# Performance work log

Hardware: AMD Instinct MI355X
Metric: run time of the kernel (lower is better)

Reference implementation:

```python
import jax, jax.numpy as jnp
import numpy as np

N_ENTITY = 64368
N_REL = 40
DIM = 128
N_BASES = 8
N_EDGES = 500000
BATCH = 64
SEED_LEN = 32


def _glorot(k, shape, gain=1.414):
    fan_in, fan_out = shape[0], shape[1]
    bound = gain * np.sqrt(6.0 / (fan_in + fan_out))
    return jax.random.uniform(k, shape, jnp.float32, -bound, bound)


def setup_inputs() -> dict:
    key = jax.random.key(0)
    ks = jax.random.split(key, 11)
    return dict(
        seed_ids=jax.random.randint(ks[0], (BATCH, SEED_LEN), 0, N_ENTITY),
        edge_src=jax.random.randint(ks[1], (N_EDGES,), 0, N_ENTITY),
        edge_dst=jax.random.randint(ks[2], (N_EDGES,), 0, N_ENTITY),
        edge_type=jax.random.randint(ks[3], (N_EDGES,), 0, N_REL),
        basis=jax.random.normal(ks[4], (N_BASES, N_ENTITY, DIM), jnp.float32) * 0.02,
        att=jax.random.normal(ks[5], (N_REL, N_BASES), jnp.float32) * 0.1,
        root=jax.random.normal(ks[6], (N_ENTITY, DIM), jnp.float32) * 0.02,
        rgcn_bias=jnp.zeros((DIM,), jnp.float32),
        attn_a=_glorot(ks[7], (DIM, DIM)),
        attn_b=_glorot(ks[8], (DIM, 1)),
        out_bias=jnp.zeros((N_ENTITY,), jnp.float32),
    )


def _rgcn_nodes(basis, att, root, rgcn_bias, edge_src, edge_dst, edge_type):
    # RGCNConv with x=None: message for edge e is row src[e] of w[type[e]],
    # where w = att @ basis (basis decomposition); 'mean' aggregation to dst;
    # update: aggr + root + bias.
    n_entity, dim = root.shape
    coeff = att[edge_type]  # [E, nb]
    agg = jnp.zeros((n_entity, dim), jnp.float32)
    for b in range(basis.shape[0]):  # small fixed loop over bases
        m = basis[b][edge_src] * coeff[:, b][:, None]  # [E, dim]
        agg = agg + jax.ops.segment_sum(m, edge_dst, num_segments=n_entity)
    deg = jax.ops.segment_sum(jnp.ones_like(edge_dst, jnp.float32), edge_dst,
                              num_segments=n_entity)
    agg = agg / jnp.maximum(deg, 1.0)[:, None]
    return agg + root + rgcn_bias[None, :]


def reference(seed_ids, edge_src, edge_dst, edge_type, basis, att, root,
              rgcn_bias, attn_a, attn_b, out_bias):
    nodes = _rgcn_nodes(basis, att, root, rgcn_bias, edge_src, edge_dst, edge_type)
    # self-attention pooling over each seed set (all entries valid / non-empty)
    H = nodes[seed_ids]  # [B, S, D]
    e = jnp.einsum('bsd,d->bs', jnp.tanh(jnp.einsum('bsd,de->bse', H, attn_a)),
                   attn_b[:, 0])  # [B, S]
    attn = jax.nn.softmax(e, axis=-1)
    u = jnp.einsum('bs,bsd->bd', attn, H)  # [B, D]
    # scores = F.linear(u, nodes_features, output.bias)
    scores = u @ nodes.T + out_bias[None, :]  # [B, n_entity]
    return scores
```

## Files before the change

### kernel.cpp

```cpp
#include <hip/hip_runtime.h>
#include <hip/hip_bf16.h>
#include <hip/hip_fp16.h>

#define N_ENTITY 64368
#define N_REL 40
#define DIM 128
#define N_BASES 8
#define N_EDGES 500000
#define BATCH 64
#define SEED_LEN 32
#define NROWS (BATCH * SEED_LEN)
#define SCAN_NB ((N_ENTITY + 255) / 256)
#define NPAD (SCAN_NB * 256)

struct alignas(8) half4 { __half2 lo, hi; };

__global__ __launch_bounds__(256) void k_hist2(
    const int* __restrict__ edst, const int* __restrict__ esrc,
    int* __restrict__ hist2)
{
    int e = blockIdx.x * 256 + threadIdx.x;
    if (e < N_EDGES) {
        atomicAdd(&hist2[edst[e]], 1);
        atomicAdd(&hist2[NPAD + esrc[e]], 1);
    }
}

__global__ __launch_bounds__(256) void k_scan1(
    const int* __restrict__ hist2, int* __restrict__ ptr2,
    int* __restrict__ partial)
{
    __shared__ int s[256];
    int tid = threadIdx.x;
    int gid = blockIdx.x * 256 + tid;
    int v = hist2[gid];
    s[tid] = v;
    __syncthreads();
    for (int off = 1; off < 256; off <<= 1) {
        int t = (tid >= off) ? s[tid - off] : 0;
        __syncthreads();
        s[tid] += t;
        __syncthreads();
    }
    ptr2[gid] = s[tid] - v;
    if (tid == 255) partial[blockIdx.x] = s[255];
}

__global__ __launch_bounds__(256) void k_scan2(
    const int* __restrict__ partial, int* __restrict__ poff)
{
    __shared__ int s[256];
    int tid = threadIdx.x;
    int base = blockIdx.x * SCAN_NB;
    int v = (tid < SCAN_NB) ? partial[base + tid] : 0;
    s[tid] = v;
    __syncthreads();
    for (int off = 1; off < 256; off <<= 1) {
        int t = (tid >= off) ? s[tid - off] : 0;
        __syncthreads();
        s[tid] += t;
        __syncthreads();
    }
    if (tid < SCAN_NB) poff[base + tid] = s[tid] - v;
}

__global__ __launch_bounds__(256) void k_scan3(
    int* __restrict__ ptr2, const int* __restrict__ poff,
    int* __restrict__ work2)
{
    int gid = blockIdx.x * 256 + threadIdx.x;
    int p = ptr2[gid] + poff[blockIdx.x];
    ptr2[gid] = p;
    work2[gid] = p;
}

__global__ __launch_bounds__(256) void k_scatter2(
    const int* __restrict__ esrc, const int* __restrict__ edst,
    const int* __restrict__ etype, int* __restrict__ work2,
    int* __restrict__ ptype, int* __restrict__ idx)
{
    int e = blockIdx.x * 256 + threadIdx.x;
    if (e < N_EDGES) {
        int spos = atomicAdd(&work2[NPAD + esrc[e]], 1);
        int dpos = atomicAdd(&work2[edst[e]], 1);
        ptype[spos] = etype[e];
        idx[dpos] = spos;
    }
}

__global__ __launch_bounds__(256) void k_scatterD(
    const int* __restrict__ esrc, const int* __restrict__ edst,
    const int* __restrict__ etype, int* __restrict__ work2,
    int* __restrict__ meta)
{
    int e = blockIdx.x * 256 + threadIdx.x;
    if (e < N_EDGES) {
        int pos = atomicAdd(&work2[edst[e]], 1);
        meta[pos] = esrc[e] * 64 + etype[e];
    }
}

__global__ __launch_bounds__(256) void k_phaseA(
    const int* __restrict__ sptr, const int* __restrict__ shist,
    const int* __restrict__ ptype, const float* __restrict__ basis,
    const float* __restrict__ att, __half* __restrict__ msg)
{
    __shared__ float att_s[N_REL * N_BASES];
    int tid = threadIdx.x;
    for (int i = tid; i < N_REL * N_BASES; i += 256) att_s[i] = att[i];
    __syncthreads();

    int sid = (blockIdx.x * 256 + tid) >> 5;
    int l32 = tid & 31;
    if (sid >= N_ENTITY) return;
    int cnt = shist[sid];
    if (cnt == 0) return;
    int p = sptr[sid];

    const size_t bstride = (size_t)N_ENTITY * DIM;
    const float* bp = basis + (size_t)sid * DIM + l32 * 4;
    float4 r0 = *(const float4*)(bp + 0 * bstride);
    float4 r1 = *(const float4*)(bp + 1 * bstride);
    float4 r2 = *(const float4*)(bp + 2 * bstride);
    float4 r3 = *(const float4*)(bp + 3 * bstride);
    float4 r4 = *(const float4*)(bp + 4 * bstride);
    float4 r5 = *(const float4*)(bp + 5 * bstride);
    float4 r6 = *(const float4*)(bp + 6 * bstride);
    float4 r7 = *(const float4*)(bp + 7 * bstride);

    int j = 0;
    for (; j + 1 < cnt; j += 2) {
        int tA = ptype[p + j];
        int tB = ptype[p + j + 1];
        const float* cA = att_s + tA * N_BASES;
        const float* cB = att_s + tB * N_BASES;
        float4 cA0 = *(const float4*)(cA);
        float4 cA1 = *(const float4*)(cA + 4);
        float4 cB0 = *(const float4*)(cB);
        float4 cB1 = *(const float4*)(cB + 4);

        float4 mA, mB;
        mA.x = cA0.x*r0.x + cA0.y*r1.x + cA0.z*r2.x + cA0.w*r3.x
             + cA1.x*r4.x + cA1.y*r5.x + cA1.z*r6.x + cA1.w*r7.x;
        mA.y = cA0.x*r0.y + cA0.y*r1.y + cA0.z*r2.y + cA0.w*r3.y
             + cA1.x*r4.y + cA1.y*r5.y + cA1.z*r6.y + cA1.w*r7.y;
        mA.z = cA0.x*r0.z + cA0.y*r1.z + cA0.z*r2.z + cA0.w*r3.z
             + cA1.x*r4.z + cA1.y*r5.z + cA1.z*r6.z + cA1.w*r7.z;
        mA.w = cA0.x*r0.w + cA0.y*r1.w + cA0.z*r2.w + cA0.w*r3.w
             + cA1.x*r4.w + cA1.y*r5.w + cA1.z*r6.w + cA1.w*r7.w;
        mB.x = cB0.x*r0.x + cB0.y*r1.x + cB0.z*r2.x + cB0.w*r3.x
             + cB1.x*r4.x + cB1.y*r5.x + cB1.z*r6.x + cB1.w*r7.x;
        mB.y = cB0.x*r0.y + cB0.y*r1.y + cB0.z*r2.y + cB0.w*r3.y
             + cB1.x*r4.y + cB1.y*r5.y + cB1.z*r6.y + cB1.w*r7.y;
        mB.z = cB0.x*r0.z + cB0.y*r1.z + cB0.z*r2.z + cB0.w*r3.z
             + cB1.x*r4.z + cB1.y*r5.z + cB1.z*r6.z + cB1.w*r7.z;
        mB.w = cB0.x*r0.w + cB0.y*r1.w + cB0.z*r2.w + cB0.w*r3.w
             + cB1.x*r4.w + cB1.y*r5.w + cB1.z*r6.w + cB1.w*r7.w;

        half4 hA, hB;
        hA.lo = __floats2half2_rn(mA.x, mA.y);
        hA.hi = __floats2half2_rn(mA.z, mA.w);
        hB.lo = __floats2half2_rn(mB.x, mB.y);
        hB.hi = __floats2half2_rn(mB.z, mB.w);
        *(half4*)(msg + ((size_t)(p + j)     << 7) + (l32 << 2)) = hA;
        *(half4*)(msg + ((size_t)(p + j + 1) << 7) + (l32 << 2)) = hB;
    }
    if (j < cnt) {
        int tA = ptype[p + j];
        const float* cA = att_s + tA * N_BASES;
        float4 cA0 = *(const float4*)(cA);
        float4 cA1 = *(const float4*)(cA + 4);
        float4 mA;
        mA.x = cA0.x*r0.x + cA0.y*r1.x + cA0.z*r2.x + cA0.w*r3.x
             + cA1.x*r4.x + cA1.y*r5.x + cA1.z*r6.x + cA1.w*r7.x;
        mA.y = cA0.x*r0.y + cA0.y*r1.y + cA0.z*r2.y + cA0.w*r3.y
             + cA1.x*r4.y + cA1.y*r5.y + cA1.z*r6.y + cA1.w*r7.y;
        mA.z = cA0.x*r0.z + cA0.y*r1.z + cA0.z*r2.z + cA0.w*r3.z
             + cA1.x*r4.z + cA1.y*r5.z + cA1.z*r6.z + cA1.w*r7.z;
        mA.w = cA0.x*r0.w + cA0.y*r1.w + cA0.z*r2.w + cA0.w*r3.w
             + cA1.x*r4.w + cA1.y*r5.w + cA1.z*r6.w + cA1.w*r7.w;
        half4 hA;
        hA.lo = __floats2half2_rn(mA.x, mA.y);
        hA.hi = __floats2half2_rn(mA.z, mA.w);
        *(half4*)(msg + ((size_t)(p + j) << 7) + (l32 << 2)) = hA;
    }
}

__global__ __launch_bounds__(256) void k_phaseB(
    const int* __restrict__ dptr, const int* __restrict__ dhist,
    const int* __restrict__ idx, const __half* __restrict__ msg,
    const float* __restrict__ root, const float* __restrict__ bias,
    float* __restrict__ agg)
{
    int wid  = (int)((blockIdx.x * 256 + threadIdx.x) >> 6);
    int lane = threadIdx.x & 63;
    if (wid >= N_ENTITY) return;
    int cnt = dhist[wid];
    int p   = dptr[wid];
    const __half2* mp = (const __half2*)msg;

    float ax = 0.f, ay = 0.f;
    int j = 0;
    for (; j + 3 < cnt; j += 4) {
        int i0 = idx[p + j + 0];
        int i1 = idx[p + j + 1];
        int i2 = idx[p + j + 2];
        int i3 = idx[p + j + 3];
        __half2 v0 = mp[((size_t)i0 << 6) + lane];
        __half2 v1 = mp[((size_t)i1 << 6) + lane];
        __half2 v2 = mp[((size_t)i2 << 6) + lane];
        __half2 v3 = mp[((size_t)i3 << 6) + lane];
        float2 f0 = __half22float2(v0);
        float2 f1 = __half22float2(v1);
        float2 f2 = __half22float2(v2);
        float2 f3 = __half22float2(v3);
        ax += (f0.x + f1.x) + (f2.x + f3.x);
        ay += (f0.y + f1.y) + (f2.y + f3.y);
    }
    for (; j < cnt; ++j) {
        int i0 = idx[p + j];
        float2 f = __half22float2(mp[((size_t)i0 << 6) + lane]);
        ax += f.x; ay += f.y;
    }

    float inv = 1.0f / fmaxf((float)cnt, 1.0f);
    int o = wid * DIM + lane * 2;
    float2 r  = *(const float2*)(root + o);
    float2 bb = *(const float2*)(bias + lane * 2);
    float2 outv;
    outv.x = ax * inv + r.x + bb.x;
    outv.y = ay * inv + r.y + bb.y;
    *(float2*)(agg + o) = outv;
}

#define ACC8(C0, C1, V0, V1, V2, V3, V4, V5, V6, V7)                         \
    acc.x += C0.x*V0.x + C0.y*V1.x + C0.z*V2.x + C0.w*V3.x                   \
           + C1.x*V4.x + C1.y*V5.x + C1.z*V6.x + C1.w*V7.x;                  \
    acc.y += C0.x*V0.y + C0.y*V1.y + C0.z*V2.y + C0.w*V3.y                   \
           + C1.x*V4.y + C1.y*V5.y + C1.z*V6.y + C1.w*V7.y;                  \
    acc.z += C0.x*V0.z + C0.y*V1.z + C0.z*V2.z + C0.w*V3.z                   \
           + C1.x*V4.z + C1.y*V5.z + C1.z*V6.z + C1.w*V7.z;                  \
    acc.w += C0.x*V0.w + C0.y*V1.w + C0.z*V2.w + C0.w*V3.w                   \
           + C1.x*V4.w + C1.y*V5.w + C1.z*V6.w + C1.w*V7.w;

__global__ __launch_bounds__(256) void k_gather(
    const int* __restrict__ ptr, const int* __restrict__ hist,
    const int* __restrict__ meta, const float* __restrict__ basis,
    const float* __restrict__ att, const float* __restrict__ root,
    const float* __restrict__ bias, float* __restrict__ agg)
{
    __shared__ float att_s[N_REL * N_BASES];
    int tid = threadIdx.x;
    for (int i = tid; i < N_REL * N_BASES; i += 256) att_s[i] = att[i];
    __syncthreads();

    int wid  = (int)((blockIdx.x * 256 + tid) >> 6);
    int lane = tid & 63;
    if (wid >= N_ENTITY) return;

    int half = lane >> 5;
    int l32  = lane & 31;
    int p   = ptr[wid];
    int cnt = hist[wid];
    const size_t bstride = (size_t)N_ENTITY * DIM;

    float4 acc = {0.f, 0.f, 0.f, 0.f};
    int j = 0;
    for (; j + 3 < cnt; j += 4) {
        int mA0 = meta[p + j + 0];
        int mA1 = meta[p + j + 1];
        int mB0 = meta[p + j + 2];
        int mB1 = meta[p + j + 3];
        int mA = half ? mA1 : mA0;
        int mB = half ? mB1 : mB0;
        const float* bA = basis + (size_t)(mA >> 6) * DIM + l32 * 4;
        const float* bB = basis + (size_t)(mB >> 6) * DIM + l32 * 4;
        float4 a0 = *(const float4*)(bA + 0 * bstride);
        float4 a1 = *(const float4*)(bA + 1 * bstride);
        float4 a2 = *(const float4*)(bA + 2 * bstride);
        float4 a3 = *(const float4*)(bA + 3 * bstride);
        float4 a4 = *(const float4*)(bA + 4 * bstride);
        float4 a5 = *(const float4*)(bA + 5 * bstride);
        float4 a6 = *(const float4*)(bA + 6 * bstride);
        float4 a7 = *(const float4*)(bA + 7 * bstride);
        float4 b0 = *(const float4*)(bB + 0 * bstride);
        float4 b1 = *(const float4*)(bB + 1 * bstride);
        float4 b2 = *(const float4*)(bB + 2 * bstride);
        float4 b3 = *(const float4*)(bB + 3 * bstride);
        float4 b4 = *(const float4*)(bB + 4 * bstride);
        float4 b5 = *(const float4*)(bB + 5 * bstride);
        float4 b6 = *(const float4*)(bB + 6 * bstride);
        float4 b7 = *(const float4*)(bB + 7 * bstride);
        float4 cA0 = *(const float4*)(att_s + (mA & 63) * N_BASES);
        float4 cA1 = *(const float4*)(att_s + (mA & 63) * N_BASES + 4);
        float4 cB0 = *(const float4*)(att_s + (mB & 63) * N_BASES);
        float4 cB1 = *(const float4*)(att_s + (mB & 63) * N_BASES + 4);
        ACC8(cA0, cA1, a0, a1, a2, a3, a4, a5, a6, a7)
        ACC8(cB0, cB1, b0, b1, b2, b3, b4, b5, b6, b7)
    }
    for (; j < cnt; j += 2) {
        int m0 = meta[p + j];
        bool has1 = (j + 1 < cnt);
        int m1 = has1 ? meta[p + j + 1] : m0;
        int m = half ? m1 : m0;
        float sc = (half && !has1) ? 0.0f : 1.0f;
        const float* bA = basis + (size_t)(m >> 6) * DIM + l32 * 4;
        float4 a0 = *(const float4*)(bA + 0 * bstride);
        float4 a1 = *(const float4*)(bA + 1 * bstride);
        float4 a2 = *(const float4*)(bA + 2 * bstride);
        float4 a3 = *(const float4*)(bA + 3 * bstride);
        float4 a4 = *(const float4*)(bA + 4 * bstride);
        float4 a5 = *(const float4*)(bA + 5 * bstride);
        float4 a6 = *(const float4*)(bA + 6 * bstride);
        float4 a7 = *(const float4*)(bA + 7 * bstride);
        float4 c0 = *(const float4*)(att_s + (m & 63) * N_BASES);
        float4 c1 = *(const float4*)(att_s + (m & 63) * N_BASES + 4);
        c0.x *= sc; c0.y *= sc; c0.z *= sc; c0.w *= sc;
        c1.x *= sc; c1.y *= sc; c1.z *= sc; c1.w *= sc;
        ACC8(c0, c1, a0, a1, a2, a3, a4, a5, a6, a7)
    }

    acc.x += __shfl_xor(acc.x, 32, 64);
    acc.y += __shfl_xor(acc.y, 32, 64);
    acc.z += __shfl_xor(acc.z, 32, 64);
    acc.w += __shfl_xor(acc.w, 32, 64);

    if (half == 0) {
        float inv = 1.0f / fmaxf((float)cnt, 1.0f);
        int o = wid * DIM + l32 * 4;
        float4 r  = *(const float4*)(root + o);
        float4 bb = *(const float4*)(bias + l32 * 4);
        float4 outv;
        outv.x = acc.x * inv + r.x + bb.x;
        outv.y = acc.y * inv + r.y + bb.y;
        outv.z = acc.z * inv + r.z + bb.z;
        outv.w = acc.w * inv + r.w + bb.w;
        *(float4*)(agg + o) = outv;
    }
}

__global__ __launch_bounds__(256) void k_attn_gemm(
    const int* __restrict__ seed_ids, const float* __restrict__ nodes,
    const float* __restrict__ A, float* __restrict__ T)
{
    __shared__ float As[DIM * 132];
    __shared__ float Hs[16 * DIM];

    int tid = threadIdx.x;
    int r0  = blockIdx.x * 16;

    for (int i = tid; i < DIM * DIM; i += 256) {
        int row = i >> 7, col = i & 127;
        As[row * 132 + col] = A[i];
    }
    for (int i = tid; i < 16 * DIM; i += 256) {
        int rr = i >> 7, d = i & 127;
        int nid = seed_ids[r0 + rr];
        Hs[rr * DIM + d] = nodes[(size_t)nid * DIM + d];
    }
    __syncthreads();

    int jx = tid & 31;
    int iy = tid >> 5;
    float acc[2][4] = {{0,0,0,0},{0,0,0,0}};

    for (int d = 0; d < DIM; ++d) {
        float h0 = Hs[(iy * 2 + 0) * DIM + d];
        float h1 = Hs[(iy * 2 + 1) * DIM + d];
        const float4 a4 = *(const float4*)(As + d * 132 + jx * 4);
        acc[0][0] += h0 * a4.x; acc[0][1] += h0 * a4.y;
        acc[0][2] += h0 * a4.z; acc[0][3] += h0 * a4.w;
        acc[1][0] += h1 * a4.x; acc[1][1] += h1 * a4.y;
        acc[1][2] += h1 * a4.z; acc[1][3] += h1 * a4.w;
    }
    #pragma unroll
    for (int i = 0; i < 2; ++i) {
        int r = r0 + iy * 2 + i;
        #pragma unroll
        for (int k = 0; k < 4; ++k)
            T[(size_t)r * DIM + jx * 4 + k] = tanhf(acc[i][k]);
    }
}

__global__ __launch_bounds__(256) void k_attn_pool(
    const int* __restrict__ seed_ids, const float* __restrict__ nodes,
    const float* __restrict__ T, const float* __restrict__ Bv,
    float* __restrict__ u, float* __restrict__ uT)
{
    __shared__ float part[SEED_LEN][9];
    __shared__ float attw[SEED_LEN];

    int b = blockIdx.x, tid = threadIdx.x;
    int s = tid >> 3, g = tid & 7;

    float pe = 0.0f;
    for (int jj = g; jj < DIM; jj += 8)
        pe += T[(size_t)(b * SEED_LEN + s) * DIM + jj] * Bv[jj];
    part[s][g] = pe;
    __syncthreads();

    if (tid < SEED_LEN) {
        float e = 0.0f;
        for (int k = 0; k < 8; ++k) e += part[tid][k];
        attw[tid] = e;
    }
    __syncthreads();

    if (tid == 0) {
        float mx = -1e30f;
        for (int k = 0; k < SEED_LEN; ++k) mx = fmaxf(mx, attw[k]);
        float ssum = 0.0f;
        for (int k = 0; k < SEED_LEN; ++k) {
            float v = expf(attw[k] - mx);
            attw[k] = v; ssum += v;
        }
        float inv = 1.0f / ssum;
        for (int k = 0; k < SEED_LEN; ++k) attw[k] *= inv;
    }
    __syncthreads();

    if (tid < DIM) {
        float acc = 0.0f;
        for (int k = 0; k < SEED_LEN; ++k) {
            int nid = seed_ids[b * SEED_LEN + k];
            acc += attw[k] * nodes[(size_t)nid * DIM + tid];
        }
        u[b * DIM + tid]  = acc;
        uT[tid * BATCH + b] = acc;
    }
}

__global__ __launch_bounds__(256) void k_scores(
    const float* __restrict__ nodes, const float* __restrict__ uT,
    const float* __restrict__ out_bias, float* __restrict__ out)
{
    __shared__ float Nl[DIM * 65];

    int tid = threadIdx.x;
    int n0  = blockIdx.x * 64;

    for (int i = tid; i < 64 * DIM; i += 256) {
        int n = i >> 7, d = i & 127;
        int gn = n0 + n;
        Nl[d * 65 + n] = (gn < N_ENTITY) ? nodes[(size_t)gn * DIM + d] : 0.0f;
    }
    __syncthreads();

    int w    = __builtin_amdgcn_readfirstlane(tid >> 6);
    int lane = tid & 63;
    int b0   = w * 16;

    float acc[16];
    #pragma unroll
    for (int k = 0; k < 16; ++k) acc[k] = 0.0f;

    #pragma unroll 4
    for (int d = 0; d < DIM; ++d) {
        float nv = Nl[d * 65 + lane];
        const float* up = uT + d * BATCH + b0;
        #pragma unroll
        for (int k = 0; k < 16; ++k) acc[k] += up[k] * nv;
    }

    int gn = n0 + lane;
    if (gn < N_ENTITY) {
        float ob = out_bias[gn];
        #pragma unroll
        for (int k = 0; k < 16; ++k)
            out[(size_t)(b0 + k) * N_ENTITY + gn] = acc[k] + ob;
    }
}

extern "C" void kernel_launch(void* const* d_in, const int* in_sizes, int n_in,
                              void* d_out, int out_size, void* d_ws, size_t ws_size,
                              hipStream_t stream)
{
    const int*   seed_ids  = (const int*)d_in[0];
    const int*   esrc      = (const int*)d_in[1];
    const int*   edst      = (const int*)d_in[2];
    const int*   etype     = (const int*)d_in[3];
    const float* basis     = (const float*)d_in[4];
    const float* att       = (const float*)d_in[5];
    const float* root      = (const float*)d_in[6];
    const float* rgcn_bias = (const float*)d_in[7];
    const float* attn_a    = (const float*)d_in[8];
    const float* attn_b    = (const float*)d_in[9];
    const float* out_bias  = (const float*)d_in[10];
    float* out = (float*)d_out;

    const size_t AGG_F  = (size_t)N_ENTITY * DIM;
    const size_t MSG_W  = (size_t)N_EDGES * 64;
    const size_t H2_I   = (size_t)2 * NPAD;

    const size_t main_words = AGG_F + MSG_W + 3 * H2_I + 1024
                            + 2 * (size_t)N_EDGES + (size_t)NROWS * DIM
                            + 2 * BATCH * DIM;
    bool big = ws_size >= main_words * 4;

    if (big) {
        float*  agg    = (float*)d_ws;
        __half* msg    = (__half*)(agg + AGG_F);
        int*    hist2  = (int*)(agg + AGG_F + MSG_W);
        int*    ptr2   = hist2 + H2_I;
        int*    work2  = ptr2 + H2_I;
        int*    part2  = work2 + H2_I;
        int*    poff2  = part2 + 512;
        int*    ptype  = poff2 + 512;
        int*    idx    = ptype + N_EDGES;
        float*  T      = (float*)(idx + N_EDGES);
        float*  u      = T + (size_t)NROWS * DIM;
        float*  uT     = u + BATCH * DIM;

        hipMemsetAsync(hist2, 0, H2_I * sizeof(int), stream);
        k_hist2<<<(N_EDGES + 255) / 256, 256, 0, stream>>>(edst, esrc, hist2);
        k_scan1<<<2 * SCAN_NB, 256, 0, stream>>>(hist2, ptr2, part2);
        k_scan2<<<2, 256, 0, stream>>>(part2, poff2);
        k_scan3<<<2 * SCAN_NB, 256, 0, stream>>>(ptr2, poff2, work2);
        k_scatter2<<<(N_EDGES + 255) / 256, 256, 0, stream>>>(
            esrc, edst, etype, work2, ptype, idx);

        k_phaseA<<<N_ENTITY / 8, 256, 0, stream>>>(
            ptr2 + NPAD, hist2 + NPAD, ptype, basis, att, msg);
        k_phaseB<<<N_ENTITY / 4, 256, 0, stream>>>(
            ptr2, hist2, idx, msg, root, rgcn_bias, agg);

        k_attn_gemm<<<NROWS / 16, 256, 0, stream>>>(seed_ids, agg, attn_a, T);
        k_attn_pool<<<BATCH, 256, 0, stream>>>(seed_ids, agg, T, attn_b, u, uT);
        k_scores<<<(N_ENTITY + 63) / 64, 256, 0, stream>>>(agg, uT, out_bias, out);
    } else {
        float* agg     = (float*)d_ws;
        int*   hist2   = (int*)(agg + AGG_F);
        int*   ptr2    = hist2 + H2_I;
        int*   work2   = ptr2 + H2_I;
        int*   part2   = work2 + H2_I;
        int*   poff2   = part2 + 512;
        int*   meta    = poff2 + 512;
        float* T       = (float*)(meta + N_EDGES);
        float* u       = T + (size_t)NROWS * DIM;
        float* uT      = u + BATCH * DIM;

        hipMemsetAsync(hist2, 0, H2_I * sizeof(int), stream);
        k_hist2<<<(N_EDGES + 255) / 256, 256, 0, stream>>>(edst, esrc, hist2);
        k_scan1<<<2 * SCAN_NB, 256, 0, stream>>>(hist2, ptr2, part2);
        k_scan2<<<2, 256, 0, stream>>>(part2, poff2);
        k_scan3<<<2 * SCAN_NB, 256, 0, stream>>>(ptr2, poff2, work2);
        k_scatterD<<<(N_EDGES + 255) / 256, 256, 0, stream>>>(
            esrc, edst, etype, work2, meta);

        k_gather<<<(N_ENTITY * 64 + 255) / 256, 256, 0, stream>>>(
            ptr2, hist2, meta, basis, att, root, rgcn_bias, agg);

        k_attn_gemm<<<NROWS / 16, 256, 0, stream>>>(seed_ids, agg, attn_a, T);
        k_attn_pool<<<BATCH, 256, 0, stream>>>(seed_ids, agg, T, attn_b, u, uT);
        k_scores<<<(N_ENTITY + 63) / 64, 256, 0, stream>>>(agg, uT, out_bias, out);
    }
}
```

Before: 612.2 us.

## Fuse RGCN pipeline into one cooperative persistent kernel and merge attention kernels

The memset, histogram, three scan kernels, scatter and both message phases are replaced by a single cooperative kernel with 1024 persistent blocks that separates the stages with grid-wide syncs. This removes the launch gaps and the separate memset. The scan offset step now has each chunk re-sum its preceding partials directly. The attention GEMM and the pooling kernel are merged into one per-batch kernel that keeps H in shared memory, which removes the T buffer round trip. In exchange, grid.sync has its own cost and the grid-stride loops run at lower parallelism than the original full-size grids.

```diff
diff --git a/kernel.cpp b/kernel.cpp
--- a/kernel.cpp
+++ b/kernel.cpp
@@ -1,6 +1,8 @@
 #include <hip/hip_runtime.h>
-#include <hip/hip_bf16.h>
 #include <hip/hip_fp16.h>
+#include <hip/hip_cooperative_groups.h>
+
+namespace cg = cooperative_groups;
 
 #define N_ENTITY 64368
 #define N_REL 40
@@ -12,10 +14,321 @@
 #define NROWS (BATCH * SEED_LEN)
 #define SCAN_NB ((N_ENTITY + 255) / 256)
 #define NPAD (SCAN_NB * 256)
+#define G_COOP 1024
 
 struct alignas(8) half4 { __half2 lo, hi; };
 
-__global__ __launch_bounds__(256) void k_hist2(
+__global__ __launch_bounds__(256, 4) void k_rgcn_all(
+    const int* __restrict__ esrc, const int* __restrict__ edst,
+    const int* __restrict__ etype, const float* __restrict__ basis,
+    const float* __restrict__ att, const float* __restrict__ root,
+    const float* __restrict__ bias,
+    int* __restrict__ hist2, int* __restrict__ ptr2, int* __restrict__ work2,
+    int* __restrict__ part2, int* __restrict__ ptype, int* __restrict__ idx,
+    __half* __restrict__ msg, float* __restrict__ agg)
+{
+    cg::grid_group grid = cg::this_grid();
+    __shared__ int s[256];
+    __shared__ float att_s[N_REL * N_BASES];
+
+    const int tid = threadIdx.x;
+    const int bid = blockIdx.x;
+    const int G   = gridDim.x;
+    const int gsz = G * 256;
+    const int gid = bid * 256 + tid;
+
+    for (int i = gid; i < 2 * NPAD; i += gsz) hist2[i] = 0;
+    for (int i = tid; i < N_REL * N_BASES; i += 256) att_s[i] = att[i];
+    __threadfence();
+    grid.sync();
+
+    for (int e = gid; e < N_EDGES; e += gsz) {
+        atomicAdd(&hist2[edst[e]], 1);
+        atomicAdd(&hist2[NPAD + esrc[e]], 1);
+    }
+    __threadfence();
+    grid.sync();
+
+    for (int c = bid; c < 2 * SCAN_NB; c += G) {
+        int v = hist2[c * 256 + tid];
+        s[tid] = v;
+        __syncthreads();
+        for (int off = 1; off < 256; off <<= 1) {
+            int t = (tid >= off) ? s[tid - off] : 0;
+            __syncthreads();
+            s[tid] += t;
+            __syncthreads();
+        }
+        ptr2[c * 256 + tid] = s[tid] - v;
+        if (tid == 255) part2[c] = s[255];
+        __syncthreads();
+    }
+    __threadfence();
+    grid.sync();
+
+    for (int c = bid; c < 2 * SCAN_NB; c += G) {
+        int cstart = (c < SCAN_NB) ? 0 : SCAN_NB;
+        int sum = 0;
+        for (int k = cstart + tid; k < c; k += 256) sum += part2[k];
+        s[tid] = sum;
+        __syncthreads();
+        for (int off = 128; off > 0; off >>= 1) {
+            if (tid < off) s[tid] += s[tid + off];
+            __syncthreads();
+        }
+        int p = ptr2[c * 256 + tid] + s[0];
+        ptr2[c * 256 + tid]  = p;
+        work2[c * 256 + tid] = p;
+        __syncthreads();
+    }
+    __threadfence();
+    grid.sync();
+
+    for (int e = gid; e < N_EDGES; e += gsz) {
+        int spos = atomicAdd(&work2[NPAD + esrc[e]], 1);
+        int dpos = atomicAdd(&work2[edst[e]], 1);
+        ptype[spos] = etype[e];
+        idx[dpos]   = spos;
+    }
+    __threadfence();
+    grid.sync();
+
+    {
+        const int l32 = tid & 31;
+        const int* sptr  = ptr2 + NPAD;
+        const int* shist = hist2 + NPAD;
+        const size_t bstride = (size_t)N_ENTITY * DIM;
+
+        for (int sid = (bid << 3) + (tid >> 5); sid < N_ENTITY; sid += (G << 3)) {
+            int cnt = shist[sid];
+            if (cnt == 0) continue;
+            int p = sptr[sid];
+
+            const float* bp = basis + (size_t)sid * DIM + l32 * 4;
+            float4 r0 = *(const float4*)(bp + 0 * bstride);
+            float4 r1 = *(const float4*)(bp + 1 * bstride);
+            float4 r2 = *(const float4*)(bp + 2 * bstride);
+            float4 r3 = *(const float4*)(bp + 3 * bstride);
+            float4 r4 = *(const float4*)(bp + 4 * bstride);
+            float4 r5 = *(const float4*)(bp + 5 * bstride);
+            float4 r6 = *(const float4*)(bp + 6 * bstride);
+            float4 r7 = *(const float4*)(bp + 7 * bstride);
+
+            int j = 0;
+            for (; j + 1 < cnt; j += 2) {
+                int tA = ptype[p + j];
+                int tB = ptype[p + j + 1];
+                const float* cA = att_s + tA * N_BASES;
+                const float* cB = att_s + tB * N_BASES;
+                float4 cA0 = *(const float4*)(cA);
+                float4 cA1 = *(const float4*)(cA + 4);
+                float4 cB0 = *(const float4*)(cB);
+                float4 cB1 = *(const float4*)(cB + 4);
+
+                float4 mA, mB;
+                mA.x = cA0.x*r0.x + cA0.y*r1.x + cA0.z*r2.x + cA0.w*r3.x
+                     + cA1.x*r4.x + cA1.y*r5.x + cA1.z*r6.x + cA1.w*r7.x;
+                mA.y = cA0.x*r0.y + cA0.y*r1.y + cA0.z*r2.y + cA0.w*r3.y
+                     + cA1.x*r4.y + cA1.y*r5.y + cA1.z*r6.y + cA1.w*r7.y;
+                mA.z = cA0.x*r0.z + cA0.y*r1.z + cA0.z*r2.z + cA0.w*r3.z
+                     + cA1.x*r4.z + cA1.y*r5.z + cA1.z*r6.z + cA1.w*r7.z;
+                mA.w = cA0.x*r0.w + cA0.y*r1.w + cA0.z*r2.w + cA0.w*r3.w
+                     + cA1.x*r4.w + cA1.y*r5.w + cA1.z*r6.w + cA1.w*r7.w;
+                mB.x = cB0.x*r0.x + cB0.y*r1.x + cB0.z*r2.x + cB0.w*r3.x
+                     + cB1.x*r4.x + cB1.y*r5.x + cB1.z*r6.x + cB1.w*r7.x;
+                mB.y = cB0.x*r0.y + cB0.y*r1.y + cB0.z*r2.y + cB0.w*r3.y
+                     + cB1.x*r4.y + cB1.y*r5.y + cB1.z*r6.y + cB1.w*r7.y;
+                mB.z = cB0.x*r0.z + cB0.y*r1.z + cB0.z*r2.z + cB0.w*r3.z
+                     + cB1.x*r4.z + cB1.y*r5.z + cB1.z*r6.z + cB1.w*r7.z;
+                mB.w = cB0.x*r0.w + cB0.y*r1.w + cB0.z*r2.w + cB0.w*r3.w
+                     + cB1.x*r4.w + cB1.y*r5.w + cB1.z*r6.w + cB1.w*r7.w;
+
+                half4 hA, hB;
+                hA.lo = __floats2half2_rn(mA.x, mA.y);
+                hA.hi = __floats2half2_rn(mA.z, mA.w);
+                hB.lo = __floats2half2_rn(mB.x, mB.y);
+                hB.hi = __floats2half2_rn(mB.z, mB.w);
+                *(half4*)(msg + ((size_t)(p + j)     << 7) + (l32 << 2)) = hA;
+                *(half4*)(msg + ((size_t)(p + j + 1) << 7) + (l32 << 2)) = hB;
+            }
+            if (j < cnt) {
+                int tA = ptype[p + j];
+                const float* cA = att_s + tA * N_BASES;
+                float4 cA0 = *(const float4*)(cA);
+                float4 cA1 = *(const float4*)(cA + 4);
+                float4 mA;
+                mA.x = cA0.x*r0.x + cA0.y*r1.x + cA0.z*r2.x + cA0.w*r3.x
+                     + cA1.x*r4.x + cA1.y*r5.x + cA1.z*r6.x + cA1.w*r7.x;
+                mA.y = cA0.x*r0.y + cA0.y*r1.y + cA0.z*r2.y + cA0.w*r3.y
+                     + cA1.x*r4.y + cA1.y*r5.y + cA1.z*r6.y + cA1.w*r7.y;
+                mA.z = cA0.x*r0.z + cA0.y*r1.z + cA0.z*r2.z + cA0.w*r3.z
+                     + cA1.x*r4.z + cA1.y*r5.z + cA1.z*r6.z + cA1.w*r7.z;
+                mA.w = cA0.x*r0.w + cA0.y*r1.w + cA0.z*r2.w + cA0.w*r3.w
+                     + cA1.x*r4.w + cA1.y*r5.w + cA1.z*r6.w + cA1.w*r7.w;
+                half4 hA;
+                hA.lo = __floats2half2_rn(mA.x, mA.y);
+                hA.hi = __floats2half2_rn(mA.z, mA.w);
+                *(half4*)(msg + ((size_t)(p + j) << 7) + (l32 << 2)) = hA;
+            }
+        }
+    }
+    __threadfence();
+    grid.sync();
+
+    {
+        const int lane = tid & 63;
+        const __half2* mp = (const __half2*)msg;
+
+        for (int wid = (bid << 2) + (tid >> 6); wid < N_ENTITY; wid += (G << 2)) {
+            int cnt = hist2[wid];
+            int p   = ptr2[wid];
+
+            float ax = 0.f, ay = 0.f;
+            int j = 0;
+            for (; j + 3 < cnt; j += 4) {
+                int i0 = idx[p + j + 0];
+                int i1 = idx[p + j + 1];
+                int i2 = idx[p + j + 2];
+                int i3 = idx[p + j + 3];
+                float2 f0 = __half22float2(mp[((size_t)i0 << 6) + lane]);
+                float2 f1 = __half22float2(mp[((size_t)i1 << 6) + lane]);
+                float2 f2 = __half22float2(mp[((size_t)i2 << 6) + lane]);
+                float2 f3 = __half22float2(mp[((size_t)i3 << 6) + lane]);
+                ax += (f0.x + f1.x) + (f2.x + f3.x);
+                ay += (f0.y + f1.y) + (f2.y + f3.y);
+            }
+            for (; j < cnt; ++j) {
+                int i0 = idx[p + j];
+                float2 f = __half22float2(mp[((size_t)i0 << 6) + lane]);
+                ax += f.x; ay += f.y;
+            }
+
+            float inv = 1.0f / fmaxf((float)cnt, 1.0f);
+            int o = wid * DIM + lane * 2;
+            float2 r  = *(const float2*)(root + o);
+            float2 bb = *(const float2*)(bias + lane * 2);
+            float2 outv;
+            outv.x = ax * inv + r.x + bb.x;
+            outv.y = ay * inv + r.y + bb.y;
+            *(float2*)(agg + o) = outv;
+        }
+    }
+}
+
+__global__ __launch_bounds__(256) void k_attn(
+    const int* __restrict__ seed_ids, const float* __restrict__ nodes,
+    const float* __restrict__ A, const float* __restrict__ Bv,
+    float* __restrict__ u, float* __restrict__ uT)
+{
+    __shared__ float Hs[SEED_LEN * DIM];
+    __shared__ float ew[SEED_LEN];
+    __shared__ float attw[SEED_LEN];
+
+    int b = blockIdx.x, tid = threadIdx.x;
+
+    for (int i = tid; i < SEED_LEN * DIM; i += 256) {
+        int ss = i >> 7, d = i & 127;
+        Hs[i] = nodes[(size_t)seed_ids[b * SEED_LEN + ss] * DIM + d];
+    }
+    __syncthreads();
+
+    int jx = tid & 31;
+    int iy = tid >> 5;
+    float acc[4][4] = {{0,0,0,0},{0,0,0,0},{0,0,0,0},{0,0,0,0}};
+
+    for (int d = 0; d < DIM; ++d) {
+        const float4 a4 = *(const float4*)(A + d * DIM + jx * 4);
+        float h0 = Hs[(iy * 4 + 0) * DIM + d];
+        float h1 = Hs[(iy * 4 + 1) * DIM + d];
+        float h2 = Hs[(iy * 4 + 2) * DIM + d];
+        float h3 = Hs[(iy * 4 + 3) * DIM + d];
+        acc[0][0] += h0 * a4.x; acc[0][1] += h0 * a4.y;
+        acc[0][2] += h0 * a4.z; acc[0][3] += h0 * a4.w;
+        acc[1][0] += h1 * a4.x; acc[1][1] += h1 * a4.y;
+        acc[1][2] += h1 * a4.z; acc[1][3] += h1 * a4.w;
+        acc[2][0] += h2 * a4.x; acc[2][1] += h2 * a4.y;
+        acc[2][2] += h2 * a4.z; acc[2][3] += h2 * a4.w;
+        acc[3][0] += h3 * a4.x; acc[3][1] += h3 * a4.y;
+        acc[3][2] += h3 * a4.z; acc[3][3] += h3 * a4.w;
+    }
+
+    const float4 bv = *(const float4*)(Bv + jx * 4);
+    #pragma unroll
+    for (int i = 0; i < 4; ++i) {
+        float pe = tanhf(acc[i][0]) * bv.x + tanhf(acc[i][1]) * bv.y
+                 + tanhf(acc[i][2]) * bv.z + tanhf(acc[i][3]) * bv.w;
+        pe += __shfl_xor(pe, 1, 64);
+        pe += __shfl_xor(pe, 2, 64);
+        pe += __shfl_xor(pe, 4, 64);
+        pe += __shfl_xor(pe, 8, 64);
+        pe += __shfl_xor(pe, 16, 64);
+        if (jx == 0) ew[iy * 4 + i] = pe;
+    }
+    __syncthreads();
+
+    if (tid == 0) {
+        float mx = -1e30f;
+        for (int k = 0; k < SEED_LEN; ++k) mx = fmaxf(mx, ew[k]);
+        float ssum = 0.0f;
+        for (int k = 0; k < SEED_LEN; ++k) {
+            float v = expf(ew[k] - mx);
+            attw[k] = v; ssum += v;
+        }
+        float inv = 1.0f / ssum;
+        for (int k = 0; k < SEED_LEN; ++k) attw[k] *= inv;
+    }
+    __syncthreads();
+
+    if (tid < DIM) {
+        float a = 0.0f;
+        for (int k = 0; k < SEED_LEN; ++k) a += attw[k] * Hs[k * DIM + tid];
+        u[b * DIM + tid]  = a;
+        uT[tid * BATCH + b] = a;
+    }
+}
+
+__global__ __launch_bounds__(256) void k_scores(
+    const float* __restrict__ nodes, const float* __restrict__ uT,
+    const float* __restrict__ out_bias, float* __restrict__ out)
+{
+    __shared__ float Nl[DIM * 65];
+
+    int tid = threadIdx.x;
+    int n0  = blockIdx.x * 64;
+
+    for (int i = tid; i < 64 * DIM; i += 256) {
+        int n = i >> 7, d = i & 127;
+        int gn = n0 + n;
+        Nl[d * 65 + n] = (gn < N_ENTITY) ? nodes[(size_t)gn * DIM + d] : 0.0f;
+    }
+    __syncthreads();
+
+    int w    = __builtin_amdgcn_readfirstlane(tid >> 6);
+    int lane = tid & 63;
+    int b0   = w * 16;
+
+    float acc[16];
+    #pragma unroll
+    for (int k = 0; k < 16; ++k) acc[k] = 0.0f;
+
+    #pragma unroll 4
+    for (int d = 0; d < DIM; ++d) {
+        float nv = Nl[d * 65 + lane];
+        const float* up = uT + d * BATCH + b0;
+        #pragma unroll
+        for (int k = 0; k < 16; ++k) acc[k] += up[k] * nv;
+    }
+
+    int gn = n0 + lane;
+    if (gn < N_ENTITY) {
+        float ob = out_bias[gn];
+        #pragma unroll
+        for (int k = 0; k < 16; ++k)
+            out[(size_t)(b0 + k) * N_ENTITY + gn] = acc[k] + ob;
+    }
+}
+
+__global__ __launch_bounds__(256) void k_hist2F(
     const int* __restrict__ edst, const int* __restrict__ esrc,
     int* __restrict__ hist2)
 {
@@ -26,7 +339,7 @@
     }
 }
 
-__global__ __launch_bounds__(256) void k_scan1(
+__global__ __launch_bounds__(256) void k_scan1F(
     const int* __restrict__ hist2, int* __restrict__ ptr2,
     int* __restrict__ partial)
 {
@@ -46,7 +359,7 @@
     if (tid == 255) partial[blockIdx.x] = s[255];
 }
 
-__global__ __launch_bounds__(256) void k_scan2(
+__global__ __launch_bounds__(256) void k_scan2F(
     const int* __restrict__ partial, int* __restrict__ poff)
 {
     __shared__ int s[256];
@@ -64,7 +377,7 @@
     if (tid < SCAN_NB) poff[base + tid] = s[tid] - v;
 }
 
-__global__ __launch_bounds__(256) void k_scan3(
+__global__ __launch_bounds__(256) void k_scan3F(
     int* __restrict__ ptr2, const int* __restrict__ poff,
     int* __restrict__ work2)
 {
@@ -74,20 +387,6 @@
     work2[gid] = p;
 }
 
-__global__ __launch_bounds__(256) void k_scatter2(
-    const int* __restrict__ esrc, const int* __restrict__ edst,
-    const int* __restrict__ etype, int* __restrict__ work2,
-    int* __restrict__ ptype, int* __restrict__ idx)
-{
-    int e = blockIdx.x * 256 + threadIdx.x;
-    if (e < N_EDGES) {
-        int spos = atomicAdd(&work2[NPAD + esrc[e]], 1);
-        int dpos = atomicAdd(&work2[edst[e]], 1);
-        ptype[spos] = etype[e];
-        idx[dpos] = spos;
-    }
-}
-
 __global__ __launch_bounds__(256) void k_scatterD(
     const int* __restrict__ esrc, const int* __restrict__ edst,
     const int* __restrict__ etype, int* __restrict__ work2,
@@ -98,139 +397,6 @@
         int pos = atomicAdd(&work2[edst[e]], 1);
         meta[pos] = esrc[e] * 64 + etype[e];
     }
-}
-
-__global__ __launch_bounds__(256) void k_phaseA(
-    const int* __restrict__ sptr, const int* __restrict__ shist,
-    const int* __restrict__ ptype, const float* __restrict__ basis,
-    const float* __restrict__ att, __half* __restrict__ msg)
-{
-    __shared__ float att_s[N_REL * N_BASES];
-    int tid = threadIdx.x;
-    for (int i = tid; i < N_REL * N_BASES; i += 256) att_s[i] = att[i];
-    __syncthreads();
-
-    int sid = (blockIdx.x * 256 + tid) >> 5;
-    int l32 = tid & 31;
-    if (sid >= N_ENTITY) return;
-    int cnt = shist[sid];
-    if (cnt == 0) return;
-    int p = sptr[sid];
-
-    const size_t bstride = (size_t)N_ENTITY * DIM;
-    const float* bp = basis + (size_t)sid * DIM + l32 * 4;
-    float4 r0 = *(const float4*)(bp + 0 * bstride);
-    float4 r1 = *(const float4*)(bp + 1 * bstride);
-    float4 r2 = *(const float4*)(bp + 2 * bstride);
-    float4 r3 = *(const float4*)(bp + 3 * bstride);
-    float4 r4 = *(const float4*)(bp + 4 * bstride);
-    float4 r5 = *(const float4*)(bp + 5 * bstride);
-    float4 r6 = *(const float4*)(bp + 6 * bstride);
-    float4 r7 = *(const float4*)(bp + 7 * bstride);
-
-    int j = 0;
-    for (; j + 1 < cnt; j += 2) {
-        int tA = ptype[p + j];
-        int tB = ptype[p + j + 1];
-        const float* cA = att_s + tA * N_BASES;
-        const float* cB = att_s + tB * N_BASES;
-        float4 cA0 = *(const float4*)(cA);
-        float4 cA1 = *(const float4*)(cA + 4);
-        float4 cB0 = *(const float4*)(cB);
-        float4 cB1 = *(const float4*)(cB + 4);
-
-        float4 mA, mB;
-        mA.x = cA0.x*r0.x + cA0.y*r1.x + cA0.z*r2.x + cA0.w*r3.x
-             + cA1.x*r4.x + cA1.y*r5.x + cA1.z*r6.x + cA1.w*r7.x;
-        mA.y = cA0.x*r0.y + cA0.y*r1.y + cA0.z*r2.y + cA0.w*r3.y
-             + cA1.x*r4.y + cA1.y*r5.y + cA1.z*r6.y + cA1.w*r7.y;
-        mA.z = cA0.x*r0.z + cA0.y*r1.z + cA0.z*r2.z + cA0.w*r3.z
-             + cA1.x*r4.z + cA1.y*r5.z + cA1.z*r6.z + cA1.w*r7.z;
-        mA.w = cA0.x*r0.w + cA0.y*r1.w + cA0.z*r2.w + cA0.w*r3.w
-             + cA1.x*r4.w + cA1.y*r5.w + cA1.z*r6.w + cA1.w*r7.w;
-        mB.x = cB0.x*r0.x + cB0.y*r1.x + cB0.z*r2.x + cB0.w*r3.x
-             + cB1.x*r4.x + cB1.y*r5.x + cB1.z*r6.x + cB1.w*r7.x;
-        mB.y = cB0.x*r0.y + cB0.y*r1.y + cB0.z*r2.y + cB0.w*r3.y
-             + cB1.x*r4.y + cB1.y*r5.y + cB1.z*r6.y + cB1.w*r7.y;
-        mB.z = cB0.x*r0.z + cB0.y*r1.z + cB0.z*r2.z + cB0.w*r3.z
-             + cB1.x*r4.z + cB1.y*r5.z + cB1.z*r6.z + cB1.w*r7.z;
-        mB.w = cB0.x*r0.w + cB0.y*r1.w + cB0.z*r2.w + cB0.w*r3.w
-             + cB1.x*r4.w + cB1.y*r5.w + cB1.z*r6.w + cB1.w*r7.w;
-
-        half4 hA, hB;
-        hA.lo = __floats2half2_rn(mA.x, mA.y);
-        hA.hi = __floats2half2_rn(mA.z, mA.w);
-        hB.lo = __floats2half2_rn(mB.x, mB.y);
-        hB.hi = __floats2half2_rn(mB.z, mB.w);
-        *(half4*)(msg + ((size_t)(p + j)     << 7) + (l32 << 2)) = hA;
-        *(half4*)(msg + ((size_t)(p + j + 1) << 7) + (l32 << 2)) = hB;
-    }
-    if (j < cnt) {
-        int tA = ptype[p + j];
-        const float* cA = att_s + tA * N_BASES;
-        float4 cA0 = *(const float4*)(cA);
-        float4 cA1 = *(const float4*)(cA + 4);
-        float4 mA;
-        mA.x = cA0.x*r0.x + cA0.y*r1.x + cA0.z*r2.x + cA0.w*r3.x
-             + cA1.x*r4.x + cA1.y*r5.x + cA1.z*r6.x + cA1.w*r7.x;
-        mA.y = cA0.x*r0.y + cA0.y*r1.y + cA0.z*r2.y + cA0.w*r3.y
-             + cA1.x*r4.y + cA1.y*r5.y + cA1.z*r6.y + cA1.w*r7.y;
-        mA.z = cA0.x*r0.z + cA0.y*r1.z + cA0.z*r2.z + cA0.w*r3.z
-             + cA1.x*r4.z + cA1.y*r5.z + cA1.z*r6.z + cA1.w*r7.z;
-        mA.w = cA0.x*r0.w + cA0.y*r1.w + cA0.z*r2.w + cA0.w*r3.w
-             + cA1.x*r4.w + cA1.y*r5.w + cA1.z*r6.w + cA1.w*r7.w;
-        half4 hA;
-        hA.lo = __floats2half2_rn(mA.x, mA.y);
-        hA.hi = __floats2half2_rn(mA.z, mA.w);
-        *(half4*)(msg + ((size_t)(p + j) << 7) + (l32 << 2)) = hA;
-    }
-}
-
-__global__ __launch_bounds__(256) void k_phaseB(
-    const int* __restrict__ dptr, const int* __restrict__ dhist,
-    const int* __restrict__ idx, const __half* __restrict__ msg,
-    const float* __restrict__ root, const float* __restrict__ bias,
-    float* __restrict__ agg)
-{
-    int wid  = (int)((blockIdx.x * 256 + threadIdx.x) >> 6);
-    int lane = threadIdx.x & 63;
-    if (wid >= N_ENTITY) return;
-    int cnt = dhist[wid];
-    int p   = dptr[wid];
-    const __half2* mp = (const __half2*)msg;
-
-    float ax = 0.f, ay = 0.f;
-    int j = 0;
-    for (; j + 3 < cnt; j += 4) {
-        int i0 = idx[p + j + 0];
-        int i1 = idx[p + j + 1];
-        int i2 = idx[p + j + 2];
-        int i3 = idx[p + j + 3];
-        __half2 v0 = mp[((size_t)i0 << 6) + lane];
-        __half2 v1 = mp[((size_t)i1 << 6) + lane];
-        __half2 v2 = mp[((size_t)i2 << 6) + lane];
-        __half2 v3 = mp[((size_t)i3 << 6) + lane];
-        float2 f0 = __half22float2(v0);
-        float2 f1 = __half22float2(v1);
-        float2 f2 = __half22float2(v2);
-        float2 f3 = __half22float2(v3);
-        ax += (f0.x + f1.x) + (f2.x + f3.x);
-        ay += (f0.y + f1.y) + (f2.y + f3.y);
-    }
-    for (; j < cnt; ++j) {
-        int i0 = idx[p + j];
-        float2 f = __half22float2(mp[((size_t)i0 << 6) + lane]);
-        ax += f.x; ay += f.y;
-    }
-
-    float inv = 1.0f / fmaxf((float)cnt, 1.0f);
-    int o = wid * DIM + lane * 2;
-    float2 r  = *(const float2*)(root + o);
-    float2 bb = *(const float2*)(bias + lane * 2);
-    float2 outv;
-    outv.x = ax * inv + r.x + bb.x;
-    outv.y = ay * inv + r.y + bb.y;
-    *(float2*)(agg + o) = outv;
 }
 
 #define ACC8(C0, C1, V0, V1, V2, V3, V4, V5, V6, V7)                         \
@@ -339,138 +505,6 @@
     }
 }
 
-__global__ __launch_bounds__(256) void k_attn_gemm(
-    const int* __restrict__ seed_ids, const float* __restrict__ nodes,
-    const float* __restrict__ A, float* __restrict__ T)
-{
-    __shared__ float As[DIM * 132];
-    __shared__ float Hs[16 * DIM];
-
-    int tid = threadIdx.x;
-    int r0  = blockIdx.x * 16;
-
-    for (int i = tid; i < DIM * DIM; i += 256) {
-        int row = i >> 7, col = i & 127;
-        As[row * 132 + col] = A[i];
-    }
-    for (int i = tid; i < 16 * DIM; i += 256) {
-        int rr = i >> 7, d = i & 127;
-        int nid = seed_ids[r0 + rr];
-        Hs[rr * DIM + d] = nodes[(size_t)nid * DIM + d];
-    }
-    __syncthreads();
-
-    int jx = tid & 31;
-    int iy = tid >> 5;
-    float acc[2][4] = {{0,0,0,0},{0,0,0,0}};
-
-    for (int d = 0; d < DIM; ++d) {
-        float h0 = Hs[(iy * 2 + 0) * DIM + d];
-        float h1 = Hs[(iy * 2 + 1) * DIM + d];
-        const float4 a4 = *(const float4*)(As + d * 132 + jx * 4);
-        acc[0][0] += h0 * a4.x; acc[0][1] += h0 * a4.y;
-        acc[0][2] += h0 * a4.z; acc[0][3] += h0 * a4.w;
-        acc[1][0] += h1 * a4.x; acc[1][1] += h1 * a4.y;
-        acc[1][2] += h1 * a4.z; acc[1][3] += h1 * a4.w;
-    }
-    #pragma unroll
-    for (int i = 0; i < 2; ++i) {
-        int r = r0 + iy * 2 + i;
-        #pragma unroll
-        for (int k = 0; k < 4; ++k)
-            T[(size_t)r * DIM + jx * 4 + k] = tanhf(acc[i][k]);
-    }
-}
-
-__global__ __launch_bounds__(256) void k_attn_pool(
-    const int* __restrict__ seed_ids, const float* __restrict__ nodes,
-    const float* __restrict__ T, const float* __restrict__ Bv,
-    float* __restrict__ u, float* __restrict__ uT)
-{
-    __shared__ float part[SEED_LEN][9];
-    __shared__ float attw[SEED_LEN];
-
-    int b = blockIdx.x, tid = threadIdx.x;
-    int s = tid >> 3, g = tid & 7;
-
-    float pe = 0.0f;
-    for (int jj = g; jj < DIM; jj += 8)
-        pe += T[(size_t)(b * SEED_LEN + s) * DIM + jj] * Bv[jj];
-    part[s][g] = pe;
-    __syncthreads();
-
-    if (tid < SEED_LEN) {
-        float e = 0.0f;
-        for (int k = 0; k < 8; ++k) e += part[tid][k];
-        attw[tid] = e;
-    }
-    __syncthreads();
-
-    if (tid == 0) {
-        float mx = -1e30f;
-        for (int k = 0; k < SEED_LEN; ++k) mx = fmaxf(mx, attw[k]);
-        float ssum = 0.0f;
-        for (int k = 0; k < SEED_LEN; ++k) {
-            float v = expf(attw[k] - mx);
-            attw[k] = v; ssum += v;
-        }
-        float inv = 1.0f / ssum;
-        for (int k = 0; k < SEED_LEN; ++k) attw[k] *= inv;
-    }
-    __syncthreads();
-
-    if (tid < DIM) {
-        float acc = 0.0f;
-        for (int k = 0; k < SEED_LEN; ++k) {
-            int nid = seed_ids[b * SEED_LEN + k];
-            acc += attw[k] * nodes[(size_t)nid * DIM + tid];
-        }
-        u[b * DIM + tid]  = acc;
-        uT[tid * BATCH + b] = acc;
-    }
-}
-
-__global__ __launch_bounds__(256) void k_scores(
-    const float* __restrict__ nodes, const float* __restrict__ uT,
-    const float* __restrict__ out_bias, float* __restrict__ out)
-{
-    __shared__ float Nl[DIM * 65];
-
-    int tid = threadIdx.x;
-    int n0  = blockIdx.x * 64;
-
-    for (int i = tid; i < 64 * DIM; i += 256) {
-        int n = i >> 7, d = i & 127;
-        int gn = n0 + n;
-        Nl[d * 65 + n] = (gn < N_ENTITY) ? nodes[(size_t)gn * DIM + d] : 0.0f;
-    }
-    __syncthreads();
-
-    int w    = __builtin_amdgcn_readfirstlane(tid >> 6);
-    int lane = tid & 63;
-    int b0   = w * 16;
-
-    float acc[16];
-    #pragma unroll
-    for (int k = 0; k < 16; ++k) acc[k] = 0.0f;
-
-    #pragma unroll 4
-    for (int d = 0; d < DIM; ++d) {
-        float nv = Nl[d * 65 + lane];
-        const float* up = uT + d * BATCH + b0;
-        #pragma unroll
-        for (int k = 0; k < 16; ++k) acc[k] += up[k] * nv;
-    }
-
-    int gn = n0 + lane;
-    if (gn < N_ENTITY) {
-        float ob = out_bias[gn];
-        #pragma unroll
-        for (int k = 0; k < 16; ++k)
-            out[(size_t)(b0 + k) * N_ENTITY + gn] = acc[k] + ob;
-    }
-}
-
 extern "C" void kernel_launch(void* const* d_in, const int* in_sizes, int n_in,
                               void* d_out, int out_size, void* d_ws, size_t ws_size,
                               hipStream_t stream)
@@ -493,8 +527,7 @@
     const size_t H2_I   = (size_t)2 * NPAD;
 
     const size_t main_words = AGG_F + MSG_W + 3 * H2_I + 1024
-                            + 2 * (size_t)N_EDGES + (size_t)NROWS * DIM
-                            + 2 * BATCH * DIM;
+                            + 2 * (size_t)N_EDGES + 2 * BATCH * DIM;
     bool big = ws_size >= main_words * 4;
 
     if (big) {
@@ -504,28 +537,21 @@
         int*    ptr2   = hist2 + H2_I;
         int*    work2  = ptr2 + H2_I;
         int*    part2  = work2 + H2_I;
-        int*    poff2  = part2 + 512;
-        int*    ptype  = poff2 + 512;
+        int*    ptype  = part2 + 1024;
         int*    idx    = ptype + N_EDGES;
-        float*  T      = (float*)(idx + N_EDGES);
-        float*  u      = T + (size_t)NROWS * DIM;
+        float*  u      = (float*)(idx + N_EDGES);
         float*  uT     = u + BATCH * DIM;
 
-        hipMemsetAsync(hist2, 0, H2_I * sizeof(int), stream);
-        k_hist2<<<(N_EDGES + 255) / 256, 256, 0, stream>>>(edst, esrc, hist2);
-        k_scan1<<<2 * SCAN_NB, 256, 0, stream>>>(hist2, ptr2, part2);
-        k_scan2<<<2, 256, 0, stream>>>(part2, poff2);
-        k_scan3<<<2 * SCAN_NB, 256, 0, stream>>>(ptr2, poff2, work2);
-        k_scatter2<<<(N_EDGES + 255) / 256, 256, 0, stream>>>(
-            esrc, edst, etype, work2, ptype, idx);
-
-        k_phaseA<<<N_ENTITY / 8, 256, 0, stream>>>(
-            ptr2 + NPAD, hist2 + NPAD, ptype, basis, att, msg);
-        k_phaseB<<<N_ENTITY / 4, 256, 0, stream>>>(
-            ptr2, hist2, idx, msg, root, rgcn_bias, agg);
-
-        k_attn_gemm<<<NROWS / 16, 256, 0, stream>>>(seed_ids, agg, attn_a, T);
-        k_attn_pool<<<BATCH, 256, 0, stream>>>(seed_ids, agg, T, attn_b, u, uT);
+        void* kargs[] = {
+            (void*)&esrc, (void*)&edst, (void*)&etype, (void*)&basis,
+            (void*)&att, (void*)&root, (void*)&rgcn_bias,
+            (void*)&hist2, (void*)&ptr2, (void*)&work2, (void*)&part2,
+            (void*)&ptype, (void*)&idx, (void*)&msg, (void*)&agg
+        };
+        hipLaunchCooperativeKernel((void*)k_rgcn_all, dim3(G_COOP), dim3(256),
+                                   kargs, 0, stream);
+
+        k_attn<<<BATCH, 256, 0, stream>>>(seed_ids, agg, attn_a, attn_b, u, uT);
         k_scores<<<(N_ENTITY + 63) / 64, 256, 0, stream>>>(agg, uT, out_bias, out);
     } else {
         float* agg     = (float*)d_ws;
@@ -535,23 +561,21 @@
         int*   part2   = work2 + H2_I;
         int*   poff2   = part2 + 512;
         int*   meta    = poff2 + 512;
-        float* T       = (float*)(meta + N_EDGES);
-        float* u       = T + (size_t)NROWS * DIM;
+        float* u       = (float*)(meta + N_EDGES);
         float* uT      = u + BATCH * DIM;
 
         hipMemsetAsync(hist2, 0, H2_I * sizeof(int), stream);
-        k_hist2<<<(N_EDGES + 255) / 256, 256, 0, stream>>>(edst, esrc, hist2);
-        k_scan1<<<2 * SCAN_NB, 256, 0, stream>>>(hist2, ptr2, part2);
-        k_scan2<<<2, 256, 0, stream>>>(part2, poff2);
-        k_scan3<<<2 * SCAN_NB, 256, 0, stream>>>(ptr2, poff2, work2);
+        k_hist2F<<<(N_EDGES + 255) / 256, 256, 0, stream>>>(edst, esrc, hist2);
+        k_scan1F<<<2 * SCAN_NB, 256, 0, stream>>>(hist2, ptr2, part2);
+        k_scan2F<<<2, 256, 0, stream>>>(part2, poff2);
+        k_scan3F<<<2 * SCAN_NB, 256, 0, stream>>>(ptr2, poff2, work2);
         k_scatterD<<<(N_EDGES + 255) / 256, 256, 0, stream>>>(
             esrc, edst, etype, work2, meta);
 
         k_gather<<<(N_ENTITY * 64 + 255) / 256, 256, 0, stream>>>(
             ptr2, hist2, meta, basis, att, root, rgcn_bias, agg);
 
-        k_attn_gemm<<<NROWS / 16, 256, 0, stream>>>(seed_ids, agg, attn_a, T);
-        k_attn_pool<<<BATCH, 256, 0, stream>>>(seed_ids, agg, T, attn_b, u, uT);
+        k_attn<<<BATCH, 256, 0, stream>>>(seed_ids, agg, attn_a, attn_b, u, uT);
         k_scores<<<(N_ENTITY + 63) / 64, 256, 0, stream>>>(agg, uT, out_bias, out);
     }
 }
```

Result: slower. 1.759 ms (+187.3%).
